# Kernel tuning notes

Hardware: AMD Instinct MI355X
Metric: run time of the kernel (lower is better)

Reference implementation:

```python
import jax, jax.numpy as jnp
import numpy as np

B, C, HW, S, G = 256, 512, 16, 256, 32
EPS = 1e-5


def setup_inputs() -> dict:
    key = jax.random.key(0)
    ks = jax.random.split(key, 6)
    scale = 0.02
    return {
        "x": jax.random.normal(ks[0], (B, C, HW, HW), dtype=jnp.float32),
        "gn_w": jnp.ones((C,), dtype=jnp.float32),
        "gn_b": jnp.zeros((C,), dtype=jnp.float32),
        "wq": jax.random.normal(ks[1], (C, C), dtype=jnp.float32) * scale,
        "bq": jnp.zeros((C,), dtype=jnp.float32),
        "wk": jax.random.normal(ks[2], (C, C), dtype=jnp.float32) * scale,
        "bk": jnp.zeros((C,), dtype=jnp.float32),
        "wv": jax.random.normal(ks[3], (C, C), dtype=jnp.float32) * scale,
        "bv": jnp.zeros((C,), dtype=jnp.float32),
        "wp": jax.random.normal(ks[4], (C, C), dtype=jnp.float32) * scale,
        "bp": jnp.zeros((C,), dtype=jnp.float32),
    }


def reference(x, gn_w, gn_b, wq, bq, wk, bk, wv, bv, wp, bp):
    b = x.shape[0]
    # GroupNorm(32, 512): normalize over (channels-in-group, H, W)
    xg = x.reshape(b, G, C // G, HW, HW)
    mu = jnp.mean(xg, axis=(2, 3, 4), keepdims=True)
    var = jnp.var(xg, axis=(2, 3, 4), keepdims=True)
    h = ((xg - mu) * jax.lax.rsqrt(var + EPS)).reshape(b, C, HW, HW)
    h = h * gn_w[:, None, None] + gn_b[:, None, None]
    hf = h.reshape(b, C, S)  # [B, C, S] with S = H*W = 256
    # 1x1 convs == per-pixel linear projections
    q = jnp.einsum('oc,bcs->bos', wq, hf) + bq[:, None]
    k = jnp.einsum('oc,bcs->bos', wk, hf) + bk[:, None]
    v = jnp.einsum('oc,bcs->bos', wv, hf) + bv[:, None]
    # w[b,s,t] = sum_c q[b,c,s] k[b,c,t]; scaled by sqrt(C)=sqrt(512) per source
    att = jnp.einsum('bcs,bct->bst', q, k) / jnp.sqrt(jnp.float32(C))
    att = jax.nn.softmax(att, axis=2)
    # torch: bmm(v, att.permute(0,2,1)) -> out[b,c,t] = sum_s v[b,c,s] att[b,t,s]
    o = jnp.einsum('bcs,bts->bct', v, att)
    o = o.reshape(b, C, HW, HW)
    o = jnp.einsum('oc,bchw->bohw', wp, o) + bp[None, :, None, None]
    return x + o
```

## Files before the change

### kernel.cpp

```cpp
#include <hip/hip_runtime.h>

typedef __attribute__((ext_vector_type(8))) short short8;
typedef __attribute__((ext_vector_type(8))) unsigned short us8;
typedef __attribute__((ext_vector_type(4))) unsigned short us4;
typedef __attribute__((ext_vector_type(4))) float f32x4;

static __device__ __forceinline__ unsigned short f2bf(float f) {
  union { float f; unsigned u; } c; c.f = f;
  unsigned r = (c.u + 0x7FFFu + ((c.u >> 16) & 1u)) >> 16;
  return (unsigned short)r;
}
static __device__ __forceinline__ float b2f(unsigned short h) {
  union { unsigned u; float f; } c; c.u = ((unsigned)h) << 16; return c.f;
}

static __device__ __forceinline__ void gll16(const unsigned short* g, unsigned short* l) {
  __builtin_amdgcn_global_load_lds(
      (const __attribute__((address_space(1))) unsigned int*)g,
      (__attribute__((address_space(3))) unsigned int*)l, 16, 0, 0);
}

__global__ __launch_bounds__(256) void conv_k(
    const float* __restrict__ wv, const float* __restrict__ wp,
    unsigned short* __restrict__ wvb, unsigned short* __restrict__ wpb)
{
  int i4 = (blockIdx.x * 256 + threadIdx.x) * 4;
  const float* src;
  unsigned short* dst;
  if (i4 < 262144) { src = wv + i4; dst = wvb + i4; }
  else             { src = wp + (i4 - 262144); dst = wpb + (i4 - 262144); }
  f32x4 v = *(const f32x4*)src;
  us4 o;
  #pragma unroll
  for (int j = 0; j < 4; ++j) o[j] = f2bf(v[j]);
  *(us4*)dst = o;
}

__global__ __launch_bounds__(256) void tk(
    const float* __restrict__ wq, const float* __restrict__ wk,
    unsigned short* __restrict__ wqT, unsigned short* __restrict__ wkT)
{
  __shared__ float L[64][65];
  const float* src = blockIdx.z ? wk : wq;
  unsigned short* dst = blockIdx.z ? wkT : wqT;
  const int ro = blockIdx.x * 64, co = blockIdx.y * 64;
  const int tid = threadIdx.x;
  #pragma unroll
  for (int p = 0; p < 4; ++p) {
    int lin = p * 1024 + tid * 4;
    int r = lin >> 6, cl = lin & 63;
    *(f32x4*)&L[r][cl] = *(const f32x4*)(src + (size_t)(ro + r) * 512 + co + cl);
  }
  __syncthreads();
  #pragma unroll
  for (int p = 0; p < 4; ++p) {
    int lin = p * 1024 + tid * 4;
    int rr = lin >> 6, cc = lin & 63;
    us4 o;
    #pragma unroll
    for (int j = 0; j < 4; ++j) o[j] = f2bf(L[cc + j][rr]);
    *(us4*)(dst + (size_t)(co + rr) * 512 + ro + cc) = o;
  }
}

__global__ __launch_bounds__(256) void w2b_k(
    const unsigned short* __restrict__ wkT, const float* __restrict__ bq,
    float* __restrict__ w2b)
{
  const int wv_ = threadIdx.x >> 6, lane = threadIdx.x & 63;
  for (int i = 0; i < 16; ++i) {
    const int c = blockIdx.x * 64 + i * 4 + wv_;
    us8 kv = *(const us8*)(wkT + (size_t)c * 512 + lane * 8);
    float s = 0.f;
    #pragma unroll
    for (int j = 0; j < 8; ++j) s += b2f(kv[j]) * bq[lane * 8 + j];
    #pragma unroll
    for (int o = 32; o; o >>= 1) s += __shfl_xor(s, o);
    if (lane == 0) w2b[c] = s;
  }
}

__global__ __launch_bounds__(512) void gn_k(
    const float* __restrict__ x, const float* __restrict__ gw,
    const float* __restrict__ gb, unsigned short* __restrict__ hT)
{
  __shared__ unsigned short tile[32][256];
  __shared__ float rs[2][4][2];
  const int b = blockIdx.x >> 4, gp = blockIdx.x & 15;
  const int tid = threadIdx.x;
  const int sub = tid >> 8;
  const int t = tid & 255;
  const int g = gp * 2 + sub;
  const float* xp = x + ((size_t)b * 512 + g * 16) * 256;
  f32x4 vals[4];
  float s = 0.f, s2 = 0.f;
  #pragma unroll
  for (int j = 0; j < 4; ++j) {
    f32x4 v = *(const f32x4*)(xp + j * 1024 + t * 4);
    vals[j] = v;
    s  += v[0] + v[1] + v[2] + v[3];
    s2 += v[0]*v[0] + v[1]*v[1] + v[2]*v[2] + v[3]*v[3];
  }
  #pragma unroll
  for (int o = 32; o; o >>= 1) { s += __shfl_xor(s, o); s2 += __shfl_xor(s2, o); }
  if ((t & 63) == 0) { rs[sub][t >> 6][0] = s; rs[sub][t >> 6][1] = s2; }
  __syncthreads();
  s  = rs[sub][0][0] + rs[sub][1][0] + rs[sub][2][0] + rs[sub][3][0];
  s2 = rs[sub][0][1] + rs[sub][1][1] + rs[sub][2][1] + rs[sub][3][1];
  const float mean = s * (1.f / 4096.f);
  const float var  = s2 * (1.f / 4096.f) - mean * mean;
  const float rstd = rsqrtf(var + 1e-5f);
  #pragma unroll
  for (int j = 0; j < 4; ++j) {
    const int cl = j * 4 + (t >> 6);
    const int c = g * 16 + cl;
    const float sc = gw[c] * rstd;
    const float sh = gb[c] - mean * sc;
    f32x4 v = vals[j];
    us4 o;
    #pragma unroll
    for (int q = 0; q < 4; ++q) o[q] = f2bf(v[q] * sc + sh);
    *(us4*)&tile[sub * 16 + cl][(t & 63) * 4] = o;
  }
  __syncthreads();
  const int srow = tid >> 1, half = tid & 1;
  us8 o0, o1;
  #pragma unroll
  for (int c = 0; c < 8; ++c) o0[c] = tile[half * 16 + c][srow];
  #pragma unroll
  for (int c = 0; c < 8; ++c) o1[c] = tile[half * 16 + 8 + c][srow];
  unsigned short* dst = hT + ((size_t)b * 256 + srow) * 512 + gp * 32 + half * 16;
  *(us8*)dst = o0;
  *(us8*)(dst + 8) = o1;
}

template<int BM, int BN, int MI, int TPB, int NWN, int NTT,
         int BIAS_MODE, bool OUT_F32, bool HAS_RESID, bool NFAST,
         int SWZ = 0, bool SBA = false, int MINW = 2>
__global__ __launch_bounds__(TPB, MINW) void gemmp_k(
    const unsigned short* __restrict__ A, long long sAb, int lda,
    const unsigned short* __restrict__ B, long long sBb, int ldb,
    void* __restrict__ Cv, long long sCb, int ldc,
    const float* __restrict__ bias, const float* __restrict__ resid)
{
  constexpr int CA = BM * 8 / TPB;
  constexpr int CB = BN * 8 / TPB;
  constexpr int ASL = SBA ? BM * 64 : 2 * BM * 64;
  __shared__ unsigned short SMEM[ASL + 2 * BN * 64];
  unsigned short* AsBase = SMEM;
  unsigned short* BsBase = SMEM + ASL;
  const int tid = threadIdx.x;
  int bz, bm, bn;
  if (SWZ) {
    const int L = blockIdx.x;
    const int xcd = L & 7, j = (L >> 3) & 7, bhi = L >> 6;
    bz = bhi * 8 + xcd;
    bm = (j >> 1) * BM;
    bn = (j & 1) * BN;
  } else {
    bz = blockIdx.z;
    bm = (NFAST ? blockIdx.y : blockIdx.x) * BM;
    bn = (NFAST ? blockIdx.x : blockIdx.y) * BN;
  }
  const int lane = tid & 63, w = tid >> 6;
  const int wr = w / NWN, wc = w % NWN;
  const int lr = lane & 15, lg = lane >> 4;
  const int csw = lr & 7;
  const int ko0 = (lg ^ csw) * 8;
  const int ko1 = ((4 + lg) ^ csw) * 8;

  const unsigned short* aSrc[CA]; int aOff[CA];
  #pragma unroll
  for (int p = 0; p < CA; ++p) {
    const int id = p * TPB + tid;
    const int row = id >> 3, cc = (id & 7) ^ (row & 7);
    aSrc[p] = A + (size_t)bz * sAb + (size_t)(bm + row) * lda + cc * 8;
    aOff[p] = id * 8;
  }
  const unsigned short* bSrc[CB]; int bOff[CB];
  #pragma unroll
  for (int p = 0; p < CB; ++p) {
    const int id = p * TPB + tid;
    const int row = id >> 3, cc = (id & 7) ^ (row & 7);
    bSrc[p] = B + (size_t)bz * sBb + (size_t)(bn + row) * ldb + cc * 8;
    bOff[p] = id * 8;
  }

  f32x4 acc[MI][4];
  #pragma unroll
  for (int i = 0; i < MI; ++i)
    #pragma unroll
    for (int j = 0; j < 4; ++j) acc[i][j] = (f32x4){0.f, 0.f, 0.f, 0.f};

  #pragma unroll
  for (int p = 0; p < CA; ++p) gll16(aSrc[p], &AsBase[aOff[p]]);
  #pragma unroll
  for (int p = 0; p < CB; ++p) gll16(bSrc[p], &BsBase[bOff[p]]);
  asm volatile("s_waitcnt vmcnt(0)" ::: "memory");
  __builtin_amdgcn_s_barrier();

  #pragma unroll 2
  for (int t = 0; t < NTT; ++t) {
    if (t + 1 < NTT) {
      const int k1 = (t + 1) * 64, sl = (t + 1) & 1;
      if (!SBA) {
        #pragma unroll
        for (int p = 0; p < CA; ++p) gll16(aSrc[p] + k1, &AsBase[sl * BM * 64 + aOff[p]]);
      }
      #pragma unroll
      for (int p = 0; p < CB; ++p) gll16(bSrc[p] + k1, &BsBase[sl * BN * 64 + bOff[p]]);
    }
    const unsigned short* At = SBA ? AsBase : &AsBase[(t & 1) * BM * 64];
    const unsigned short* Bt = &BsBase[(t & 1) * BN * 64];
    short8 bf[4][2];
    #pragma unroll
    for (int nj = 0; nj < 4; ++nj) {
      bf[nj][0] = *(const short8*)(Bt + (wc * 64 + nj * 16 + lr) * 64 + ko0);
      bf[nj][1] = *(const short8*)(Bt + (wc * 64 + nj * 16 + lr) * 64 + ko1);
    }
    #pragma unroll
    for (int h = 0; h < MI / 4; ++h) {
      short8 af[4][2];
      #pragma unroll
      for (int mi = 0; mi < 4; ++mi) {
        const int rr = wr * (MI * 16) + h * 64 + mi * 16 + lr;
        af[mi][0] = *(const short8*)(At + rr * 64 + ko0);
        af[mi][1] = *(const short8*)(At + rr * 64 + ko1);
      }
      __builtin_amdgcn_s_setprio(1);
      #pragma unroll
      for (int mi = 0; mi < 4; ++mi)
        #pragma unroll
        for (int nj = 0; nj < 4; ++nj) {
          acc[h * 4 + mi][nj] = __builtin_amdgcn_mfma_f32_16x16x32_bf16(af[mi][0], bf[nj][0], acc[h * 4 + mi][nj], 0, 0, 0);
          acc[h * 4 + mi][nj] = __builtin_amdgcn_mfma_f32_16x16x32_bf16(af[mi][1], bf[nj][1], acc[h * 4 + mi][nj], 0, 0, 0);
        }
      __builtin_amdgcn_s_setprio(0);
    }
    if (t + 1 < NTT) {
      asm volatile("s_waitcnt vmcnt(0)" ::: "memory");
      __builtin_amdgcn_s_barrier();
      if (SBA) {
        const int k1 = (t + 1) * 64;
        #pragma unroll
        for (int p = 0; p < CA; ++p) gll16(aSrc[p] + k1, &AsBase[aOff[p]]);
        asm volatile("s_waitcnt vmcnt(0)" ::: "memory");
        __builtin_amdgcn_s_barrier();
      }
    }
  }

  #pragma unroll
  for (int mi = 0; mi < MI; ++mi) {
    #pragma unroll
    for (int r = 0; r < 4; ++r) {
      const int rowc = bm + wr * (MI * 16) + mi * 16 + lg * 4 + r;
      const float bv_ = (BIAS_MODE == 1) ? bias[rowc] : 0.f;
      #pragma unroll
      for (int ni = 0; ni < 4; ++ni) {
        const int col = bn + wc * 64 + ni * 16 + lr;
        float vv = acc[mi][ni][r] + bv_;
        if (BIAS_MODE == 2) vv += bias[col];
        const size_t idx = (size_t)bz * sCb + (size_t)rowc * ldc + col;
        if (HAS_RESID) vv += resid[idx];
        if (OUT_F32) ((float*)Cv)[idx] = vv;
        else ((unsigned short*)Cv)[idx] = f2bf(vv);
      }
    }
  }
}

__global__ __launch_bounds__(512, 1) void fused_k(
    const unsigned short* __restrict__ A,
    const unsigned short* __restrict__ B,
    const unsigned short* __restrict__ V,
    unsigned short* __restrict__ O)
{
  __shared__ __attribute__((aligned(16))) char SM[147456];
  unsigned short* AsB = (unsigned short*)SM;
  unsigned short* BsB = (unsigned short*)(SM + 65536);
  unsigned short* attL = (unsigned short*)SM;
  unsigned short* vbuf = (unsigned short*)(SM + 131072);
  float* redm = (float*)(SM + 131072);
  float* reds = redm + 1024;

  const int tid = threadIdx.x;
  const int bz = blockIdx.z;
  const int lane = tid & 63, w = tid >> 6;
  const int wr = w >> 2, wc = w & 3;
  const int lr = lane & 15, lg = lane >> 4;
  const int csw = lr & 7;
  const int ko0 = (lg ^ csw) * 8;
  const int ko1 = ((4 + lg) ^ csw) * 8;

  const int rl = tid >> 3;
  const int gc = (tid & 7) ^ (rl & 7);
  const unsigned short* pA = A + (size_t)bz * 131072 + (size_t)rl * 512 + gc * 8;
  const unsigned short* pB = B + (size_t)bz * 131072 + (size_t)rl * 512 + gc * 8;

  auto stageA = [&](int t, int h) {
    const unsigned short* s = pA + (size_t)h * 65536 + t * 64;
    unsigned short* d = AsB + ((2 * t + h) & 3) * 8192 + tid * 8;
    gll16(s, d);
    gll16(s + 32768, d + 4096);
  };
  auto stageB = [&](int t, int h) {
    const unsigned short* s = pB + (size_t)h * 65536 + t * 64;
    unsigned short* d = BsB + ((2 * t + h) & 3) * 8192 + tid * 8;
    gll16(s, d);
    gll16(s + 32768, d + 4096);
  };

  f32x4 acc[8][4];
  #pragma unroll
  for (int i = 0; i < 8; ++i)
    #pragma unroll
    for (int j = 0; j < 4; ++j) acc[i][j] = (f32x4){0.f, 0.f, 0.f, 0.f};

  stageA(0, 0); stageA(0, 1); stageB(0, 0); stageB(0, 1);
  stageB(1, 0); stageA(1, 0); stageA(1, 1);
  asm volatile("s_waitcnt vmcnt(6)" ::: "memory");
  __builtin_amdgcn_s_barrier();

  constexpr int NT = 8;
  for (int t = 0; t < NT; ++t) {
    const unsigned short* sA = AsB + ((2 * t + wr) & 3) * 8192;
    const unsigned short* sB = BsB + ((2 * t + (wc >> 1)) & 3) * 8192;
    const int bc = (wc & 1) * 64;
    short8 af[4][2], bf0[2][2], bf1[2][2];

    #pragma unroll
    for (int mi = 0; mi < 4; ++mi) {
      af[mi][0] = *(const short8*)(sA + (mi * 16 + lr) * 64 + ko0);
      af[mi][1] = *(const short8*)(sA + (mi * 16 + lr) * 64 + ko1);
    }
    #pragma unroll
    for (int nj = 0; nj < 2; ++nj) {
      bf0[nj][0] = *(const short8*)(sB + (bc + nj * 16 + lr) * 64 + ko0);
      bf0[nj][1] = *(const short8*)(sB + (bc + nj * 16 + lr) * 64 + ko1);
    }
    if (t + 1 < NT) stageB(t + 1, 1);
    __builtin_amdgcn_s_barrier();
    __builtin_amdgcn_s_setprio(1);
    #pragma unroll
    for (int mi = 0; mi < 4; ++mi)
      #pragma unroll
      for (int nj = 0; nj < 2; ++nj) {
        acc[mi][nj] = __builtin_amdgcn_mfma_f32_16x16x32_bf16(af[mi][0], bf0[nj][0], acc[mi][nj], 0, 0, 0);
        acc[mi][nj] = __builtin_amdgcn_mfma_f32_16x16x32_bf16(af[mi][1], bf0[nj][1], acc[mi][nj], 0, 0, 0);
      }
    __builtin_amdgcn_s_setprio(0);
    __builtin_amdgcn_s_barrier();

    #pragma unroll
    for (int nj = 0; nj < 2; ++nj) {
      bf1[nj][0] = *(const short8*)(sB + (bc + 32 + nj * 16 + lr) * 64 + ko0);
      bf1[nj][1] = *(const short8*)(sB + (bc + 32 + nj * 16 + lr) * 64 + ko1);
    }
    __builtin_amdgcn_s_barrier();
    __builtin_amdgcn_s_setprio(1);
    #pragma unroll
    for (int mi = 0; mi < 4; ++mi)
      #pragma unroll
      for (int nj = 0; nj < 2; ++nj) {
        acc[mi][2 + nj] = __builtin_amdgcn_mfma_f32_16x16x32_bf16(af[mi][0], bf1[nj][0], acc[mi][2 + nj], 0, 0, 0);
        acc[mi][2 + nj] = __builtin_amdgcn_mfma_f32_16x16x32_bf16(af[mi][1], bf1[nj][1], acc[mi][2 + nj], 0, 0, 0);
      }
    __builtin_amdgcn_s_setprio(0);
    __builtin_amdgcn_s_barrier();

    #pragma unroll
    for (int mi = 0; mi < 4; ++mi) {
      af[mi][0] = *(const short8*)(sA + (64 + mi * 16 + lr) * 64 + ko0);
      af[mi][1] = *(const short8*)(sA + (64 + mi * 16 + lr) * 64 + ko1);
    }
    if (t + 2 < NT) stageB(t + 2, 0);
    __builtin_amdgcn_s_barrier();
    __builtin_amdgcn_s_setprio(1);
    #pragma unroll
    for (int mi = 0; mi < 4; ++mi)
      #pragma unroll
      for (int nj = 0; nj < 2; ++nj) {
        acc[4 + mi][nj] = __builtin_amdgcn_mfma_f32_16x16x32_bf16(af[mi][0], bf0[nj][0], acc[4 + mi][nj], 0, 0, 0);
        acc[4 + mi][nj] = __builtin_amdgcn_mfma_f32_16x16x32_bf16(af[mi][1], bf0[nj][1], acc[4 + mi][nj], 0, 0, 0);
      }
    __builtin_amdgcn_s_setprio(0);
    __builtin_amdgcn_s_barrier();

    if (t + 2 < NT) { stageA(t + 2, 0); stageA(t + 2, 1); }
    __builtin_amdgcn_s_barrier();
    __builtin_amdgcn_s_setprio(1);
    #pragma unroll
    for (int mi = 0; mi < 4; ++mi)
      #pragma unroll
      for (int nj = 0; nj < 2; ++nj) {
        acc[4 + mi][2 + nj] = __builtin_amdgcn_mfma_f32_16x16x32_bf16(af[mi][0], bf1[nj][0], acc[4 + mi][2 + nj], 0, 0, 0);
        acc[4 + mi][2 + nj] = __builtin_amdgcn_mfma_f32_16x16x32_bf16(af[mi][1], bf1[nj][1], acc[4 + mi][2 + nj], 0, 0, 0);
      }
    __builtin_amdgcn_s_setprio(0);
    if (t == NT - 2)      asm volatile("s_waitcnt vmcnt(0)" ::: "memory");
    else if (t < NT - 2)  asm volatile("s_waitcnt vmcnt(6)" ::: "memory");
    __builtin_amdgcn_s_barrier();
  }

  const float SC = 0.044194173824159216f;
  float rmax[8][4];
  #pragma unroll
  for (int mi = 0; mi < 8; ++mi)
    #pragma unroll
    for (int r = 0; r < 4; ++r) {
      float m = fmaxf(fmaxf(acc[mi][0][r], acc[mi][1][r]),
                      fmaxf(acc[mi][2][r], acc[mi][3][r]));
      #pragma unroll
      for (int o = 1; o <= 8; o <<= 1) m = fmaxf(m, __shfl_xor(m, o));
      rmax[mi][r] = m;
    }
  __syncthreads();
  if (lr == 0) {
    #pragma unroll
    for (int mi = 0; mi < 8; ++mi)
      #pragma unroll
      for (int r = 0; r < 4; ++r)
        redm[(wr * 128 + mi * 16 + lg * 4 + r) * 4 + wc] = rmax[mi][r];
  }
  __syncthreads();
  float rsum[8][4];
  #pragma unroll
  for (int mi = 0; mi < 8; ++mi)
    #pragma unroll
    for (int r = 0; r < 4; ++r) {
      const int row = wr * 128 + mi * 16 + lg * 4 + r;
      f32x4 q = *(const f32x4*)&redm[row * 4];
      const float m = fmaxf(fmaxf(q[0], q[1]), fmaxf(q[2], q[3]));
      float s = 0.f;
      #pragma unroll
      for (int ni = 0; ni < 4; ++ni) {
        float e = __expf((acc[mi][ni][r] - m) * SC);
        acc[mi][ni][r] = e;
        s += e;
      }
      #pragma unroll
      for (int o = 1; o <= 8; o <<= 1) s += __shfl_xor(s, o);
      rsum[mi][r] = s;
    }
  if (lr == 0) {
    #pragma unroll
    for (int mi = 0; mi < 8; ++mi)
      #pragma unroll
      for (int r = 0; r < 4; ++r)
        reds[(wr * 128 + mi * 16 + lg * 4 + r) * 4 + wc] = rsum[mi][r];
  }
  __syncthreads();

  #pragma unroll
  for (int mi = 0; mi < 8; ++mi)
    #pragma unroll
    for (int r = 0; r < 4; ++r) {
      const int trow = wr * 128 + mi * 16 + lg * 4 + r;
      f32x4 q = *(const f32x4*)&reds[trow * 4];
      const float inv = 1.f / (q[0] + q[1] + q[2] + q[3]);
      const int t7 = trow & 7;
      #pragma unroll
      for (int ni = 0; ni < 4; ++ni) {
        const int cw = ni * 2 + (lr >> 3);
        const int off = trow * 256 + wc * 64 + ((cw ^ t7) << 3) + (lr & 7);
        attL[off] = f2bf(acc[mi][ni][r] * inv);
      }
    }
  __syncthreads();

  const unsigned short* Vb = V + (size_t)bz * 131072;
  unsigned short* Ob = O + (size_t)bz * 131072;
  const int vrow = tid >> 3;
  const int vgc = (tid & 7) ^ (vrow & 7);
  us8 nv0, nv1;
  auto ldV = [&](int idx) {
    const int ps = idx >> 2, kt = idx & 3;
    const unsigned short* s0 = Vb + (size_t)(ps * 128 + vrow) * 256 + kt * 64 + vgc * 8;
    nv0 = *(const us8*)s0;
    nv1 = *(const us8*)(s0 + (size_t)64 * 256);
  };
  auto stV = [&]() {
    *(us8*)(vbuf + tid * 8) = nv0;
    *(us8*)(vbuf + (512 + tid) * 8) = nv1;
  };
  ldV(0); stV();
  __syncthreads();
  for (int pass = 0; pass < 4; ++pass) {
    f32x4 po[8][2];
    #pragma unroll
    for (int i = 0; i < 8; ++i)
      #pragma unroll
      for (int j = 0; j < 2; ++j) po[i][j] = (f32x4){0.f, 0.f, 0.f, 0.f};
    for (int kt = 0; kt < 4; ++kt) {
      const int idx = pass * 4 + kt;
      if (idx + 1 < 16) ldV(idx + 1);
      short8 bfv[2][2];
      #pragma unroll
      for (int nj = 0; nj < 2; ++nj) {
        bfv[nj][0] = *(const short8*)(vbuf + (wc * 32 + nj * 16 + lr) * 64 + ko0);
        bfv[nj][1] = *(const short8*)(vbuf + (wc * 32 + nj * 16 + lr) * 64 + ko1);
      }
      __builtin_amdgcn_s_setprio(1);
      #pragma unroll
      for (int mi = 0; mi < 8; ++mi) {
        const int trow = wr * 128 + mi * 16 + lr;
        const int t7 = trow & 7;
        const unsigned short* ap = attL + trow * 256 + kt * 64;
        short8 afv0 = *(const short8*)(ap + ((lg ^ t7) << 3));
        short8 afv1 = *(const short8*)(ap + (((4 + lg) ^ t7) << 3));
        #pragma unroll
        for (int nj = 0; nj < 2; ++nj) {
          po[mi][nj] = __builtin_amdgcn_mfma_f32_16x16x32_bf16(afv0, bfv[nj][0], po[mi][nj], 0, 0, 0);
          po[mi][nj] = __builtin_amdgcn_mfma_f32_16x16x32_bf16(afv1, bfv[nj][1], po[mi][nj], 0, 0, 0);
        }
      }
      __builtin_amdgcn_s_setprio(0);
      __syncthreads();
      if (idx + 1 < 16) stV();
      __syncthreads();
    }
    #pragma unroll
    for (int mi = 0; mi < 8; ++mi)
      #pragma unroll
      for (int r = 0; r < 4; ++r) {
        const int trow = wr * 128 + mi * 16 + lg * 4 + r;
        #pragma unroll
        for (int nj = 0; nj < 2; ++nj) {
          const int c = pass * 128 + wc * 32 + nj * 16 + lr;
          Ob[(size_t)trow * 512 + c] = f2bf(po[mi][nj][r]);
        }
      }
  }
}

extern "C" void kernel_launch(void* const* d_in, const int* in_sizes, int n_in,
                              void* d_out, int out_size, void* d_ws, size_t ws_size,
                              hipStream_t stream)
{
  const float* x   = (const float*)d_in[0];
  const float* gnw = (const float*)d_in[1];
  const float* gnb = (const float*)d_in[2];
  const float* wq  = (const float*)d_in[3];
  const float* bq  = (const float*)d_in[4];
  const float* wk  = (const float*)d_in[5];
  const float* wv  = (const float*)d_in[7];
  const float* bv  = (const float*)d_in[8];
  const float* wp  = (const float*)d_in[9];
  const float* bp  = (const float*)d_in[10];
  float* out = (float*)d_out;

  char* ws = (char*)d_ws;
  unsigned short* W2T   = (unsigned short*)(ws);
  unsigned short* wvb   = (unsigned short*)(ws + 524288);
  unsigned short* wpb   = (unsigned short*)(ws + 1048576);
  unsigned short* wqT   = (unsigned short*)(ws + 1572864);
  unsigned short* wkT   = (unsigned short*)(ws + 2097152);
  float*          w2b   = (float*)(ws + 2621440);
  unsigned short* hT    = (unsigned short*)(ws + 2885632);
  unsigned short* T1    = (unsigned short*)(ws + 69994496ull);
  unsigned short* v     = (unsigned short*)(ws + 137103360ull);
  unsigned short* oT    = hT;

  conv_k<<<512, 256, 0, stream>>>(wv, wp, wvb, wpb);
  tk<<<dim3(8, 8, 2), 256, 0, stream>>>(wq, wk, wqT, wkT);
  w2b_k<<<8, 256, 0, stream>>>(wkT, bq, w2b);
  gemmp_k<128, 128, 4, 256, 2, 8, 0, false, false, false><<<dim3(4, 4, 1), 256, 0, stream>>>(
      wkT, 0, 512, wqT, 0, 512, W2T, 0, 512, nullptr, nullptr);
  gn_k<<<4096, 512, 0, stream>>>(x, gnw, gnb, hT);
  gemmp_k<256, 256, 8, 512, 4, 8, 2, false, false, true><<<dim3(2, 256, 1), 512, 0, stream>>>(
      hT, 0, 512, W2T, 0, 512, T1, 0, 512, w2b, nullptr);
  gemmp_k<128, 128, 4, 256, 2, 8, 1, false, false, false, 1, true, 3><<<dim3(2048, 1, 1), 256, 0, stream>>>(
      wvb, 0, 512, hT, 131072, 512, v, 131072, 256, bv, nullptr);
  fused_k<<<dim3(1, 1, 256), 512, 0, stream>>>(T1, hT, v, oT);
  gemmp_k<128, 128, 4, 256, 2, 8, 1, true, true, false, 1, true, 3><<<dim3(2048, 1, 1), 256, 0, stream>>>(
      wpb, 0, 512, oT, 131072, 512, out, 131072, 256, bp, x);
}
```

Before: 300.5 us.

## Fold V projection into output projection via precomputed Wp·Wv product

Removes the per-batch V projection GEMM by precomputing Wp·Wv and a folded bias Wp·bv+bp. The attention kernel now consumes the normalized activations h directly (written additionally by the GroupNorm kernel in channel-major layout) instead of v. Only the final projection GEMM with the combined weight remains. It also drops the single-buffered-A GEMM variant. The trade-off is an extra bf16 write of h, plus rounding from the bf16 product weight.

```diff
diff --git a/kernel.cpp b/kernel.cpp
--- a/kernel.cpp
+++ b/kernel.cpp
@@ -21,28 +21,25 @@
 }
 
 __global__ __launch_bounds__(256) void conv_k(
-    const float* __restrict__ wv, const float* __restrict__ wp,
-    unsigned short* __restrict__ wvb, unsigned short* __restrict__ wpb)
+    const float* __restrict__ wp, unsigned short* __restrict__ wpb)
 {
   int i4 = (blockIdx.x * 256 + threadIdx.x) * 4;
-  const float* src;
-  unsigned short* dst;
-  if (i4 < 262144) { src = wv + i4; dst = wvb + i4; }
-  else             { src = wp + (i4 - 262144); dst = wpb + (i4 - 262144); }
-  f32x4 v = *(const f32x4*)src;
+  f32x4 v = *(const f32x4*)(wp + i4);
   us4 o;
   #pragma unroll
   for (int j = 0; j < 4; ++j) o[j] = f2bf(v[j]);
-  *(us4*)dst = o;
+  *(us4*)(wpb + i4) = o;
 }
 
 __global__ __launch_bounds__(256) void tk(
     const float* __restrict__ wq, const float* __restrict__ wk,
-    unsigned short* __restrict__ wqT, unsigned short* __restrict__ wkT)
+    const float* __restrict__ wv,
+    unsigned short* __restrict__ wqT, unsigned short* __restrict__ wkT,
+    unsigned short* __restrict__ wvT)
 {
   __shared__ float L[64][65];
-  const float* src = blockIdx.z ? wk : wq;
-  unsigned short* dst = blockIdx.z ? wkT : wqT;
+  const float* src = blockIdx.z == 0 ? wq : (blockIdx.z == 1 ? wk : wv);
+  unsigned short* dst = blockIdx.z == 0 ? wqT : (blockIdx.z == 1 ? wkT : wvT);
   const int ro = blockIdx.x * 64, co = blockIdx.y * 64;
   const int tid = threadIdx.x;
   #pragma unroll
@@ -80,9 +77,30 @@
   }
 }
 
+__global__ __launch_bounds__(256) void bfold_k(
+    const float* __restrict__ wp, const float* __restrict__ bv,
+    const float* __restrict__ bp, float* __restrict__ bfold)
+{
+  const int wv_ = threadIdx.x >> 6, lane = threadIdx.x & 63;
+  for (int i = 0; i < 16; ++i) {
+    const int c = blockIdx.x * 64 + i * 4 + wv_;
+    const float* row = wp + (size_t)c * 512 + lane * 8;
+    f32x4 a0 = *(const f32x4*)row;
+    f32x4 a1 = *(const f32x4*)(row + 4);
+    f32x4 b0 = *(const f32x4*)(bv + lane * 8);
+    f32x4 b1 = *(const f32x4*)(bv + lane * 8 + 4);
+    float s = a0[0]*b0[0] + a0[1]*b0[1] + a0[2]*b0[2] + a0[3]*b0[3]
+            + a1[0]*b1[0] + a1[1]*b1[1] + a1[2]*b1[2] + a1[3]*b1[3];
+    #pragma unroll
+    for (int o = 32; o; o >>= 1) s += __shfl_xor(s, o);
+    if (lane == 0) bfold[c] = s + bp[c];
+  }
+}
+
 __global__ __launch_bounds__(512) void gn_k(
     const float* __restrict__ x, const float* __restrict__ gw,
-    const float* __restrict__ gb, unsigned short* __restrict__ hT)
+    const float* __restrict__ gb, unsigned short* __restrict__ hT,
+    unsigned short* __restrict__ h)
 {
   __shared__ unsigned short tile[32][256];
   __shared__ float rs[2][4][2];
@@ -121,6 +139,7 @@
     #pragma unroll
     for (int q = 0; q < 4; ++q) o[q] = f2bf(v[q] * sc + sh);
     *(us4*)&tile[sub * 16 + cl][(t & 63) * 4] = o;
+    *(us4*)(h + ((size_t)b * 512 + c) * 256 + (t & 63) * 4) = o;
   }
   __syncthreads();
   const int srow = tid >> 1, half = tid & 1;
@@ -135,9 +154,8 @@
 }
 
 template<int BM, int BN, int MI, int TPB, int NWN, int NTT,
-         int BIAS_MODE, bool OUT_F32, bool HAS_RESID, bool NFAST,
-         int SWZ = 0, bool SBA = false, int MINW = 2>
-__global__ __launch_bounds__(TPB, MINW) void gemmp_k(
+         int BIAS_MODE, bool OUT_F32, bool HAS_RESID, bool NFAST, int SWZ = 0>
+__global__ __launch_bounds__(TPB, 2) void gemmp_k(
     const unsigned short* __restrict__ A, long long sAb, int lda,
     const unsigned short* __restrict__ B, long long sBb, int ldb,
     void* __restrict__ Cv, long long sCb, int ldc,
@@ -145,10 +163,9 @@
 {
   constexpr int CA = BM * 8 / TPB;
   constexpr int CB = BN * 8 / TPB;
-  constexpr int ASL = SBA ? BM * 64 : 2 * BM * 64;
-  __shared__ unsigned short SMEM[ASL + 2 * BN * 64];
+  __shared__ unsigned short SMEM[2 * BM * 64 + 2 * BN * 64];
   unsigned short* AsBase = SMEM;
-  unsigned short* BsBase = SMEM + ASL;
+  unsigned short* BsBase = SMEM + 2 * BM * 64;
   const int tid = threadIdx.x;
   int bz, bm, bn;
   if (SWZ) {
@@ -203,14 +220,12 @@
   for (int t = 0; t < NTT; ++t) {
     if (t + 1 < NTT) {
       const int k1 = (t + 1) * 64, sl = (t + 1) & 1;
-      if (!SBA) {
-        #pragma unroll
-        for (int p = 0; p < CA; ++p) gll16(aSrc[p] + k1, &AsBase[sl * BM * 64 + aOff[p]]);
-      }
+      #pragma unroll
+      for (int p = 0; p < CA; ++p) gll16(aSrc[p] + k1, &AsBase[sl * BM * 64 + aOff[p]]);
       #pragma unroll
       for (int p = 0; p < CB; ++p) gll16(bSrc[p] + k1, &BsBase[sl * BN * 64 + bOff[p]]);
     }
-    const unsigned short* At = SBA ? AsBase : &AsBase[(t & 1) * BM * 64];
+    const unsigned short* At = &AsBase[(t & 1) * BM * 64];
     const unsigned short* Bt = &BsBase[(t & 1) * BN * 64];
     short8 bf[4][2];
     #pragma unroll
@@ -240,13 +255,6 @@
     if (t + 1 < NTT) {
       asm volatile("s_waitcnt vmcnt(0)" ::: "memory");
       __builtin_amdgcn_s_barrier();
-      if (SBA) {
-        const int k1 = (t + 1) * 64;
-        #pragma unroll
-        for (int p = 0; p < CA; ++p) gll16(aSrc[p] + k1, &AsBase[aOff[p]]);
-        asm volatile("s_waitcnt vmcnt(0)" ::: "memory");
-        __builtin_amdgcn_s_barrier();
-      }
     }
   }
 
@@ -552,27 +560,30 @@
 
   char* ws = (char*)d_ws;
   unsigned short* W2T   = (unsigned short*)(ws);
-  unsigned short* wvb   = (unsigned short*)(ws + 524288);
+  unsigned short* wvT   = (unsigned short*)(ws + 524288);
   unsigned short* wpb   = (unsigned short*)(ws + 1048576);
   unsigned short* wqT   = (unsigned short*)(ws + 1572864);
   unsigned short* wkT   = (unsigned short*)(ws + 2097152);
   float*          w2b   = (float*)(ws + 2621440);
-  unsigned short* hT    = (unsigned short*)(ws + 2885632);
-  unsigned short* T1    = (unsigned short*)(ws + 69994496ull);
-  unsigned short* v     = (unsigned short*)(ws + 137103360ull);
-  unsigned short* oT    = hT;
-
-  conv_k<<<512, 256, 0, stream>>>(wv, wp, wvb, wpb);
-  tk<<<dim3(8, 8, 2), 256, 0, stream>>>(wq, wk, wqT, wkT);
+  float*          bfold = (float*)(ws + 2623488);
+  unsigned short* Wpvb  = (unsigned short*)(ws + 2625536);
+  unsigned short* hT    = (unsigned short*)(ws + 3276800);
+  unsigned short* T1    = (unsigned short*)(ws + 70385664ull);
+  unsigned short* h     = (unsigned short*)(ws + 137494528ull);
+  unsigned short* yT    = hT;
+
+  conv_k<<<256, 256, 0, stream>>>(wp, wpb);
+  tk<<<dim3(8, 8, 3), 256, 0, stream>>>(wq, wk, wv, wqT, wkT, wvT);
   w2b_k<<<8, 256, 0, stream>>>(wkT, bq, w2b);
+  bfold_k<<<8, 256, 0, stream>>>(wp, bv, bp, bfold);
   gemmp_k<128, 128, 4, 256, 2, 8, 0, false, false, false><<<dim3(4, 4, 1), 256, 0, stream>>>(
       wkT, 0, 512, wqT, 0, 512, W2T, 0, 512, nullptr, nullptr);
-  gn_k<<<4096, 512, 0, stream>>>(x, gnw, gnb, hT);
+  gemmp_k<128, 128, 4, 256, 2, 8, 0, false, false, false><<<dim3(4, 4, 1), 256, 0, stream>>>(
+      wpb, 0, 512, wvT, 0, 512, Wpvb, 0, 512, nullptr, nullptr);
+  gn_k<<<4096, 512, 0, stream>>>(x, gnw, gnb, hT, h);
   gemmp_k<256, 256, 8, 512, 4, 8, 2, false, false, true><<<dim3(2, 256, 1), 512, 0, stream>>>(
       hT, 0, 512, W2T, 0, 512, T1, 0, 512, w2b, nullptr);
-  gemmp_k<128, 128, 4, 256, 2, 8, 1, false, false, false, 1, true, 3><<<dim3(2048, 1, 1), 256, 0, stream>>>(
-      wvb, 0, 512, hT, 131072, 512, v, 131072, 256, bv, nullptr);
-  fused_k<<<dim3(1, 1, 256), 512, 0, stream>>>(T1, hT, v, oT);
-  gemmp_k<128, 128, 4, 256, 2, 8, 1, true, true, false, 1, true, 3><<<dim3(2048, 1, 1), 256, 0, stream>>>(
-      wpb, 0, 512, oT, 131072, 512, out, 131072, 256, bp, x);
-}
+  fused_k<<<dim3(1, 1, 256), 512, 0, stream>>>(T1, hT, h, yT);
+  gemmp_k<128, 128, 4, 256, 2, 8, 1, true, true, false, 1><<<dim3(2048, 1, 1), 256, 0, stream>>>(
+      Wpvb, 0, 512, yT, 131072, 512, out, 131072, 256, bfold, x);
+}
```

Measured after the change: 288.3 us. -4.1%, faster.
